# Optimization experiments

Measured on AMD Instinct MI355X. Metric: run time of the kernel, lower is better.

The kernel has to match this reference:

```python
import jax, jax.numpy as jnp
import numpy as np

NB, NLOC, DIN, DOUT = 4, 4096, 512, 512
NTYPES, TEBD = 128, 128
N_EXPERTS, TOP_K = 8, 2  # share_expert = 0 -> routed_experts = 8, routed_top_k = 2


def setup_inputs() -> dict:
    key = jax.random.key(0)
    k = jax.random.split(key, 6)
    return {
        "x": jax.random.normal(k[0], (NB, NLOC, DIN), dtype=jnp.float32),
        "type_embeddings": jax.random.normal(k[1], (NTYPES, TEBD), dtype=jnp.float32),
        "atom_types": jax.random.randint(k[2], (NB, NLOC), 0, NTYPES, dtype=jnp.int32),
        "Wg": jax.random.normal(k[3], (TEBD, N_EXPERTS), dtype=jnp.float32) / np.sqrt(TEBD),
        "We": jax.random.normal(k[4], (N_EXPERTS, DIN, DOUT), dtype=jnp.float32) / np.sqrt(DIN),
        "be": jax.random.normal(k[5], (N_EXPERTS, DOUT), dtype=jnp.float32) * 0.01,
    }


def reference(x, type_embeddings, atom_types, Wg, We, be):
    # --- route: gate on type embeddings, then index per atom (MD-continuous) ---
    logits = type_embeddings @ Wg                       # [ntypes, E]
    top_vals, top_idx = jax.lax.top_k(logits, TOP_K)    # [ntypes, K]
    weights = jax.nn.softmax(top_vals, axis=-1)         # softmax over selected logits
    atom_w = weights[atom_types]                        # [nb, nloc, K]
    atom_i = top_idx[atom_types]                        # [nb, nloc, K]

    # scatter-add top-k weights into dense per-expert weights (matches scatter_add_)
    onehot = jax.nn.one_hot(atom_i, N_EXPERTS, dtype=x.dtype)   # [nb, nloc, K, E]
    per_expert_w = jnp.einsum("bnk,bnke->bne", atom_w, onehot)  # [nb, nloc, E]

    # --- run all experts densely (the batched JIT-friendly path), then combine ---
    expert_out = jnp.tanh(jnp.einsum("bnd,edo->bneo", x, We) + be)  # [nb, nloc, E, dout]
    out = jnp.einsum("bne,bneo->bno", per_expert_w, expert_out)     # [nb, nloc, dout]
    return out
```

## Files before the change

kernel.cpp:

```cpp
#include <hip/hip_runtime.h>
#include <hip/hip_bf16.h>
#include <math.h>

typedef __bf16 bf16;
typedef __bf16 bf16x8 __attribute__((ext_vector_type(8)));
typedef float  f32x4  __attribute__((ext_vector_type(4)));

#define NTOK   16384
#define DIN    512
#define DOUT   512
#define NTYPES 128
#define TEBD   128
#define NEXP   8
#define NPAIR  64
#define MAXTILE 192

#define WS_HPART   0
#define WS_ROUTE_W 32768
#define WS_BASET   33792
#define WS_CURS    34304
#define WS_CNTP    34816
#define WS_BASEP   35072
#define WS_NTILE   35328
#define WS_TMAP    35840
#define WS_RMAP    37888
#define WS_WGT     (WS_RMAP + MAXTILE * 128 * 4)
#define WS_XB      (WS_WGT + MAXTILE * 128 * 8)
#define WS_WET     (WS_XB + (size_t)NTOK * DIN * 2)

#define GLOAD_LDS16(g, l)                                                     \
  __builtin_amdgcn_global_load_lds(                                           \
      (const __attribute__((address_space(1))) void*)(g),                     \
      (__attribute__((address_space(3))) void*)(l), 16, 0, 0)

__global__ void fused_prep_kernel(const float* __restrict__ x,
                                  const float* __restrict__ We,
                                  const int* __restrict__ atype,
                                  int* __restrict__ hpart,
                                  bf16* __restrict__ xb,
                                  bf16* __restrict__ WeT) {
  int bx = blockIdx.x;
  int tid = threadIdx.x;
  if (bx < 64) {
    __shared__ int h[NTYPES];
    if (tid < NTYPES) h[tid] = 0;
    __syncthreads();
    int t = bx * 256 + tid;
    atomicAdd(&h[atype[t]], 1);
    __syncthreads();
    if (tid < NTYPES) hpart[tid * 64 + bx] = h[tid];
  } else if (bx < 576) {
    __shared__ float t[64][65];
    int b2 = bx - 64;
    int e = b2 >> 6;
    int rem = b2 & 63;
    int kt = (rem >> 3) * 64;
    int nt = (rem & 7) * 64;
    int col = tid & 63;
    int rq = tid >> 6;
#pragma unroll
    for (int r = 0; r < 16; ++r) {
      int row = rq * 16 + r;
      t[row][col] = We[((size_t)e * DIN + kt + row) * DOUT + nt + col];
    }
    __syncthreads();
#pragma unroll
    for (int r = 0; r < 16; ++r) {
      int n = rq * 16 + r;
      WeT[((size_t)e * DOUT + nt + n) * DIN + kt + col] = (bf16)t[col][n];
    }
  } else {
    size_t base = (size_t)(bx - 576) * 4096 + tid * 16;
    const float4* p = (const float4*)(x + base);
    float4 a0 = p[0], a1 = p[1], a2 = p[2], a3 = p[3];
    bf16x8 o0, o1;
    o0[0] = (bf16)a0.x; o0[1] = (bf16)a0.y; o0[2] = (bf16)a0.z; o0[3] = (bf16)a0.w;
    o0[4] = (bf16)a1.x; o0[5] = (bf16)a1.y; o0[6] = (bf16)a1.z; o0[7] = (bf16)a1.w;
    o1[0] = (bf16)a2.x; o1[1] = (bf16)a2.y; o1[2] = (bf16)a2.z; o1[3] = (bf16)a2.w;
    o1[4] = (bf16)a3.x; o1[5] = (bf16)a3.y; o1[6] = (bf16)a3.z; o1[7] = (bf16)a3.w;
    *(bf16x8*)(xb + base) = o0;
    *(bf16x8*)(xb + base + 8) = o1;
  }
}

__global__ void route_scan_kernel(const float* __restrict__ emb,
                                  const float* __restrict__ Wg,
                                  const int* __restrict__ hpart,
                                  float* __restrict__ route_w,
                                  int* __restrict__ base_type,
                                  int* __restrict__ cursor,
                                  int* __restrict__ cnt_pair,
                                  int* __restrict__ base_pair,
                                  int* __restrict__ ntile,
                                  int* __restrict__ tmap,
                                  int* __restrict__ row_map) {
  __shared__ int s_cnt[NPAIR];
  __shared__ int s_off[NTYPES];
  __shared__ int s_pair[NTYPES];
  int t = threadIdx.x;
  if (t < NPAIR) s_cnt[t] = 0;
  __syncthreads();

  int myc = 0;
  {
    const int4* hp = (const int4*)(hpart + t * 64);
#pragma unroll
    for (int b = 0; b < 16; ++b) {
      int4 v = hp[b];
      myc += v.x + v.y + v.z + v.w;
    }
  }

  const float* er = emb + (size_t)t * TEBD;
  float lg[NEXP];
#pragma unroll
  for (int e = 0; e < NEXP; ++e) lg[e] = 0.f;
  for (int j = 0; j < TEBD; ++j) {
    float ev = er[j];
#pragma unroll
    for (int e = 0; e < NEXP; ++e) lg[e] += ev * Wg[j * NEXP + e];
  }
  float v0 = -__builtin_inff(), v1 = -__builtin_inff();
  int i0 = 0, i1 = 0;
#pragma unroll
  for (int e = 0; e < NEXP; ++e) {
    float v = lg[e];
    if (v > v0) { v1 = v0; i1 = i0; v0 = v; i0 = e; }
    else if (v > v1) { v1 = v; i1 = e; }
  }
  float d = expf(v1 - v0);
  float inv = 1.f / (1.f + d);
  route_w[t * 2 + 0] = inv;
  route_w[t * 2 + 1] = d * inv;
  int p = i0 * 8 + i1;
  s_pair[t] = p;
  s_off[t] = atomicAdd(&s_cnt[p], myc);
  cursor[t] = 0;
  __syncthreads();

  if (t < NPAIR) {
    int b = 0, tb = 0;
    for (int j = 0; j < t; ++j) {
      int nt_j = (s_cnt[j] + 127) >> 7;
      b += nt_j << 7;
      tb += nt_j;
    }
    base_pair[t] = b;
    cnt_pair[t] = s_cnt[t];
    int nt_l = (s_cnt[t] + 127) >> 7;
    for (int i = 0; i < nt_l; ++i) {
      tmap[(tb + i) * 2 + 0] = t;
      tmap[(tb + i) * 2 + 1] = i * 128;
    }
    for (int i = s_cnt[t]; i < (nt_l << 7); ++i) row_map[b + i] = 0;
    if (t == NPAIR - 1) ntile[0] = tb + nt_l;
  }
  __syncthreads();
  base_type[t] = base_pair[s_pair[t]] + s_off[t];
}

__global__ void place_kernel(const int* __restrict__ atype,
                             const float* __restrict__ route_w,
                             const int* __restrict__ base_type,
                             int* __restrict__ cursor,
                             int* __restrict__ row_map,
                             float* __restrict__ wgt) {
  __shared__ int lc[NTYPES];
  __shared__ int lb[NTYPES];
  int tid = threadIdx.x;
  if (tid < NTYPES) lc[tid] = 0;
  __syncthreads();
  int t = blockIdx.x * 256 + tid;
  int ty = atype[t];
  int r = atomicAdd(&lc[ty], 1);
  __syncthreads();
  if (tid < NTYPES) lb[tid] = lc[tid] ? atomicAdd(&cursor[tid], lc[tid]) : 0;
  __syncthreads();
  int pos = base_type[ty] + lb[ty] + r;
  row_map[pos] = t;
  ((float2*)wgt)[pos] = ((const float2*)route_w)[ty];
}

__global__ __launch_bounds__(256, 2) void moe_gemm_pair_kernel(
    const bf16* __restrict__ xb, const bf16* __restrict__ WeT,
    const float* __restrict__ be, const int* __restrict__ cnt_pair,
    const int* __restrict__ ntile, const int* __restrict__ tmap,
    const int* __restrict__ row_map, const float* __restrict__ wgt,
    float* __restrict__ out) {
  int nwork = ntile[0] * 8;
  int f = blockIdx.y * 8 + blockIdx.x;
  if (f >= nwork) return;
  int q = nwork >> 3, r = nwork & 7;
  int xcd = f & 7, idx = f >> 3;
  int L = (xcd < r ? xcd * (q + 1) : r * (q + 1) + (xcd - r) * q) + idx;
  int ti = L >> 3;
  int cx = L & 7;
  int list = tmap[ti * 2 + 0];
  int r0   = tmap[ti * 2 + 1];
  int e0 = list >> 3, e1 = list & 7;
  int nrow = cnt_pair[list] - r0;
  if (nrow > 128) nrow = 128;
  int c0 = cx * 64;
  int arow0 = ti * 128;

  __shared__ __align__(16) bf16 As[4][128 * 32];
  __shared__ __align__(16) bf16 B0s[4][64 * 32];
  __shared__ __align__(16) bf16 B1s[4][64 * 32];
  __shared__ int   tokS[128];
  __shared__ float w0S[128], w1S[128];
  __shared__ float be0S[64], be1S[64];

  int tid = threadIdx.x;
  int lane = tid & 63, w = tid >> 6;

  if (tid < 128) {
    int srow = (tid < nrow) ? tid : (nrow - 1);
    tokS[tid] = row_map[arow0 + srow];
    float2 ww = ((const float2*)wgt)[arow0 + srow];
    w0S[tid] = ww.x;
    w1S[tid] = ww.y;
    if (tid < 64) {
      be0S[tid] = be[e0 * DOUT + c0 + tid];
      be1S[tid] = be[e1 * DOUT + c0 + tid];
    }
  }
  __syncthreads();

  const bf16* srcA[2];
#pragma unroll
  for (int j = 0; j < 2; ++j) {
    int slot = w * 128 + j * 64 + lane;
    int row = slot >> 2, cs = slot & 3;
    int c = cs ^ ((row >> 1) & 3);
    srcA[j] = xb + (size_t)tokS[row] * DIN + c * 8;
  }
  const bf16* srcB0;
  const bf16* srcB1;
  {
    int slot = w * 64 + lane;
    int row = slot >> 2, cs = slot & 3;
    int c = cs ^ ((row >> 1) & 3);
    srcB0 = WeT + ((size_t)e0 * DOUT + c0 + row) * DIN + c * 8;
    srcB1 = WeT + ((size_t)e1 * DOUT + c0 + row) * DIN + c * 8;
  }

  auto stage = [&](int buf) {
#pragma unroll
    for (int j = 0; j < 2; ++j) {
      GLOAD_LDS16(srcA[j], &As[buf][(w * 128 + j * 64) * 8]);
      srcA[j] += 32;
    }
    GLOAD_LDS16(srcB0, &B0s[buf][w * 64 * 8]);
    GLOAD_LDS16(srcB1, &B1s[buf][w * 64 * 8]);
    srcB0 += 32;
    srcB1 += 32;
  };

  stage(0);
  stage(1);
  stage(2);

  f32x4 acc0[4][2], acc1[4][2];
#pragma unroll
  for (int mi = 0; mi < 4; ++mi)
#pragma unroll
    for (int ni = 0; ni < 2; ++ni) { acc0[mi][ni] = (f32x4)0.f; acc1[mi][ni] = (f32x4)0.f; }

  int wm = (w >> 1) * 64;
  int wn = (w & 1) * 32;
  int r16 = lane & 15, g16 = lane >> 4;

  int offA[4], offB[2];
#pragma unroll
  for (int i = 0; i < 4; ++i) {
    int rA = wm + i * 16 + r16;
    offA[i] = rA * 32 + (g16 ^ ((rA >> 1) & 3)) * 8;
  }
#pragma unroll
  for (int i = 0; i < 2; ++i) {
    int rB = wn + i * 16 + r16;
    offB[i] = rB * 32 + (g16 ^ ((rB >> 1) & 3)) * 8;
  }

#pragma unroll
  for (int t = 0; t < 16; ++t) {
    if (t < 14)      asm volatile("s_waitcnt vmcnt(8)" ::: "memory");
    else if (t == 14) asm volatile("s_waitcnt vmcnt(4)" ::: "memory");
    else              asm volatile("s_waitcnt vmcnt(0)" ::: "memory");
    __builtin_amdgcn_s_barrier();
    if (t + 3 < 16) stage((t + 3) & 3);

    int cur = t & 3;
    bf16x8 af[4], b0f[2], b1f[2];
#pragma unroll
    for (int i = 0; i < 4; ++i) af[i] = *(const bf16x8*)&As[cur][offA[i]];
#pragma unroll
    for (int i = 0; i < 2; ++i) b0f[i] = *(const bf16x8*)&B0s[cur][offB[i]];
#pragma unroll
    for (int i = 0; i < 2; ++i) b1f[i] = *(const bf16x8*)&B1s[cur][offB[i]];
    __builtin_amdgcn_s_setprio(1);
#pragma unroll
    for (int mi = 0; mi < 4; ++mi)
#pragma unroll
      for (int ni = 0; ni < 2; ++ni) {
        acc0[mi][ni] = __builtin_amdgcn_mfma_f32_16x16x32_bf16(
            af[mi], b0f[ni], acc0[mi][ni], 0, 0, 0);
        acc1[mi][ni] = __builtin_amdgcn_mfma_f32_16x16x32_bf16(
            af[mi], b1f[ni], acc1[mi][ni], 0, 0, 0);
      }
    __builtin_amdgcn_s_setprio(0);
  }

#pragma unroll
  for (int mi = 0; mi < 4; ++mi) {
#pragma unroll
    for (int ni = 0; ni < 2; ++ni) {
      f32x4 v0 = acc0[mi][ni];
      f32x4 v1 = acc1[mi][ni];
      int colLocal = wn + ni * 16 + r16;
      float bev0 = be0S[colLocal];
      float bev1 = be1S[colLocal];
#pragma unroll
      for (int r = 0; r < 4; ++r) {
        int lrow = wm + mi * 16 + g16 * 4 + r;
        if (lrow < nrow) {
          float x0 = fminf(9.f, fmaxf(-9.f, v0[r] + bev0)) * 2.885390082f;
          float x1 = fminf(9.f, fmaxf(-9.f, v1[r] + bev1)) * 2.885390082f;
          float e0v, e1v, invd;
          asm("v_exp_f32 %0, %1" : "=v"(e0v) : "v"(x0));
          asm("v_exp_f32 %0, %1" : "=v"(e1v) : "v"(x1));
          float d0 = e0v + 1.f, d1 = e1v + 1.f;
          asm("v_rcp_f32 %0, %1" : "=v"(invd) : "v"(d0 * d1));
          float t0 = (e0v - 1.f) * d1 * invd;
          float t1 = (e1v - 1.f) * d0 * invd;
          out[(size_t)tokS[lrow] * DOUT + c0 + colLocal] =
              t0 * w0S[lrow] + t1 * w1S[lrow];
        }
      }
    }
  }
}

extern "C" void kernel_launch(void* const* d_in, const int* in_sizes, int n_in,
                              void* d_out, int out_size, void* d_ws, size_t ws_size,
                              hipStream_t stream) {
  const float* x    = (const float*)d_in[0];
  const float* emb  = (const float*)d_in[1];
  const int*   aty  = (const int*)d_in[2];
  const float* Wg   = (const float*)d_in[3];
  const float* We   = (const float*)d_in[4];
  const float* be   = (const float*)d_in[5];
  float* out = (float*)d_out;

  char* ws = (char*)d_ws;
  int*   hpart     = (int*)(ws + WS_HPART);
  float* route_w   = (float*)(ws + WS_ROUTE_W);
  int*   base_type = (int*)(ws + WS_BASET);
  int*   cursor    = (int*)(ws + WS_CURS);
  int*   cnt_pair  = (int*)(ws + WS_CNTP);
  int*   base_pair = (int*)(ws + WS_BASEP);
  int*   ntile     = (int*)(ws + WS_NTILE);
  int*   tmap      = (int*)(ws + WS_TMAP);
  int*   row_map   = (int*)(ws + WS_RMAP);
  float* wgt       = (float*)(ws + WS_WGT);
  bf16*  xb        = (bf16*)(ws + WS_XB);
  bf16*  WeT       = (bf16*)(ws + WS_WET);

  fused_prep_kernel<<<2624, 256, 0, stream>>>(x, We, aty, hpart, xb, WeT);
  route_scan_kernel<<<1, 128, 0, stream>>>(emb, Wg, hpart, route_w, base_type,
                                           cursor, cnt_pair, base_pair, ntile,
                                           tmap, row_map);
  place_kernel<<<NTOK / 256, 256, 0, stream>>>(aty, route_w, base_type, cursor,
                                               row_map, wgt);
  moe_gemm_pair_kernel<<<dim3(8, MAXTILE), 256, 0, stream>>>(
      xb, WeT, be, cnt_pair, ntile, tmap, row_map, wgt, out);
}
```

Before: 74.83 us.

## Fuse x bf16 conversion into GEMM A-tile load; drop separate x cast pass

Removes the standalone pass that converted x to bf16 in a workspace. The GEMM now loads fp32 rows of x straight into LDS and converts them to bf16 while building fragments. The We transpose moves into the placement kernel, and the histogram becomes its own small kernel. This saves a full read and write of x, but each GEMM tile now loads twice the A bytes into LDS. To fit LDS it also drops from 4 to 3 pipeline stages, which shortens the prefetch depth.

```diff
diff --git a/kernel.cpp b/kernel.cpp
--- a/kernel.cpp
+++ b/kernel.cpp
@@ -25,62 +25,22 @@
 #define WS_TMAP    35840
 #define WS_RMAP    37888
 #define WS_WGT     (WS_RMAP + MAXTILE * 128 * 4)
-#define WS_XB      (WS_WGT + MAXTILE * 128 * 8)
-#define WS_WET     (WS_XB + (size_t)NTOK * DIN * 2)
+#define WS_WET     (WS_WGT + MAXTILE * 128 * 8)
 
 #define GLOAD_LDS16(g, l)                                                     \
   __builtin_amdgcn_global_load_lds(                                           \
       (const __attribute__((address_space(1))) void*)(g),                     \
       (__attribute__((address_space(3))) void*)(l), 16, 0, 0)
 
-__global__ void fused_prep_kernel(const float* __restrict__ x,
-                                  const float* __restrict__ We,
-                                  const int* __restrict__ atype,
-                                  int* __restrict__ hpart,
-                                  bf16* __restrict__ xb,
-                                  bf16* __restrict__ WeT) {
-  int bx = blockIdx.x;
+__global__ void hist_kernel(const int* __restrict__ atype, int* __restrict__ hpart) {
+  __shared__ int h[NTYPES];
   int tid = threadIdx.x;
-  if (bx < 64) {
-    __shared__ int h[NTYPES];
-    if (tid < NTYPES) h[tid] = 0;
-    __syncthreads();
-    int t = bx * 256 + tid;
-    atomicAdd(&h[atype[t]], 1);
-    __syncthreads();
-    if (tid < NTYPES) hpart[tid * 64 + bx] = h[tid];
-  } else if (bx < 576) {
-    __shared__ float t[64][65];
-    int b2 = bx - 64;
-    int e = b2 >> 6;
-    int rem = b2 & 63;
-    int kt = (rem >> 3) * 64;
-    int nt = (rem & 7) * 64;
-    int col = tid & 63;
-    int rq = tid >> 6;
-#pragma unroll
-    for (int r = 0; r < 16; ++r) {
-      int row = rq * 16 + r;
-      t[row][col] = We[((size_t)e * DIN + kt + row) * DOUT + nt + col];
-    }
-    __syncthreads();
-#pragma unroll
-    for (int r = 0; r < 16; ++r) {
-      int n = rq * 16 + r;
-      WeT[((size_t)e * DOUT + nt + n) * DIN + kt + col] = (bf16)t[col][n];
-    }
-  } else {
-    size_t base = (size_t)(bx - 576) * 4096 + tid * 16;
-    const float4* p = (const float4*)(x + base);
-    float4 a0 = p[0], a1 = p[1], a2 = p[2], a3 = p[3];
-    bf16x8 o0, o1;
-    o0[0] = (bf16)a0.x; o0[1] = (bf16)a0.y; o0[2] = (bf16)a0.z; o0[3] = (bf16)a0.w;
-    o0[4] = (bf16)a1.x; o0[5] = (bf16)a1.y; o0[6] = (bf16)a1.z; o0[7] = (bf16)a1.w;
-    o1[0] = (bf16)a2.x; o1[1] = (bf16)a2.y; o1[2] = (bf16)a2.z; o1[3] = (bf16)a2.w;
-    o1[4] = (bf16)a3.x; o1[5] = (bf16)a3.y; o1[6] = (bf16)a3.z; o1[7] = (bf16)a3.w;
-    *(bf16x8*)(xb + base) = o0;
-    *(bf16x8*)(xb + base + 8) = o1;
-  }
+  if (tid < NTYPES) h[tid] = 0;
+  __syncthreads();
+  int t = blockIdx.x * 256 + tid;
+  atomicAdd(&h[atype[t]], 1);
+  __syncthreads();
+  if (tid < NTYPES) hpart[tid * 64 + blockIdx.x] = h[tid];
 }
 
 __global__ void route_scan_kernel(const float* __restrict__ emb,
@@ -159,30 +119,55 @@
   base_type[t] = base_pair[s_pair[t]] + s_off[t];
 }
 
-__global__ void place_kernel(const int* __restrict__ atype,
+__global__ void prep2_kernel(const float* __restrict__ We,
+                             const int* __restrict__ atype,
                              const float* __restrict__ route_w,
                              const int* __restrict__ base_type,
                              int* __restrict__ cursor,
                              int* __restrict__ row_map,
-                             float* __restrict__ wgt) {
-  __shared__ int lc[NTYPES];
-  __shared__ int lb[NTYPES];
+                             float* __restrict__ wgt,
+                             bf16* __restrict__ WeT) {
+  int bx = blockIdx.x;
   int tid = threadIdx.x;
-  if (tid < NTYPES) lc[tid] = 0;
-  __syncthreads();
-  int t = blockIdx.x * 256 + tid;
-  int ty = atype[t];
-  int r = atomicAdd(&lc[ty], 1);
-  __syncthreads();
-  if (tid < NTYPES) lb[tid] = lc[tid] ? atomicAdd(&cursor[tid], lc[tid]) : 0;
-  __syncthreads();
-  int pos = base_type[ty] + lb[ty] + r;
-  row_map[pos] = t;
-  ((float2*)wgt)[pos] = ((const float2*)route_w)[ty];
+  if (bx < 64) {
+    __shared__ int lc[NTYPES];
+    __shared__ int lb[NTYPES];
+    if (tid < NTYPES) lc[tid] = 0;
+    __syncthreads();
+    int t = bx * 256 + tid;
+    int ty = atype[t];
+    int r = atomicAdd(&lc[ty], 1);
+    __syncthreads();
+    if (tid < NTYPES) lb[tid] = lc[tid] ? atomicAdd(&cursor[tid], lc[tid]) : 0;
+    __syncthreads();
+    int pos = base_type[ty] + lb[ty] + r;
+    row_map[pos] = t;
+    ((float2*)wgt)[pos] = ((const float2*)route_w)[ty];
+  } else {
+    __shared__ float t[64][65];
+    int b2 = bx - 64;
+    int e = b2 >> 6;
+    int rem = b2 & 63;
+    int kt = (rem >> 3) * 64;
+    int nt = (rem & 7) * 64;
+    int col = tid & 63;
+    int rq = tid >> 6;
+#pragma unroll
+    for (int r = 0; r < 16; ++r) {
+      int row = rq * 16 + r;
+      t[row][col] = We[((size_t)e * DIN + kt + row) * DOUT + nt + col];
+    }
+    __syncthreads();
+#pragma unroll
+    for (int r = 0; r < 16; ++r) {
+      int n = rq * 16 + r;
+      WeT[((size_t)e * DOUT + nt + n) * DIN + kt + col] = (bf16)t[col][n];
+    }
+  }
 }
 
 __global__ __launch_bounds__(256, 2) void moe_gemm_pair_kernel(
-    const bf16* __restrict__ xb, const bf16* __restrict__ WeT,
+    const float* __restrict__ x, const bf16* __restrict__ WeT,
     const float* __restrict__ be, const int* __restrict__ cnt_pair,
     const int* __restrict__ ntile, const int* __restrict__ tmap,
     const int* __restrict__ row_map, const float* __restrict__ wgt,
@@ -203,9 +188,9 @@
   int c0 = cx * 64;
   int arow0 = ti * 128;
 
-  __shared__ __align__(16) bf16 As[4][128 * 32];
-  __shared__ __align__(16) bf16 B0s[4][64 * 32];
-  __shared__ __align__(16) bf16 B1s[4][64 * 32];
+  __shared__ __align__(16) float Asf[3][128 * 32];
+  __shared__ __align__(16) bf16  B0s[3][64 * 32];
+  __shared__ __align__(16) bf16  B1s[3][64 * 32];
   __shared__ int   tokS[128];
   __shared__ float w0S[128], w1S[128];
   __shared__ float be0S[64], be1S[64];
@@ -226,13 +211,13 @@
   }
   __syncthreads();
 
-  const bf16* srcA[2];
-#pragma unroll
-  for (int j = 0; j < 2; ++j) {
-    int slot = w * 128 + j * 64 + lane;
-    int row = slot >> 2, cs = slot & 3;
-    int c = cs ^ ((row >> 1) & 3);
-    srcA[j] = xb + (size_t)tokS[row] * DIN + c * 8;
+  const float* srcA[4];
+#pragma unroll
+  for (int j = 0; j < 4; ++j) {
+    int slot = (j * 4 + w) * 64 + lane;
+    int row = slot >> 3, cs = slot & 7;
+    int c = cs ^ (row & 7);
+    srcA[j] = x + (size_t)tokS[row] * DIN + c * 4;
   }
   const bf16* srcB0;
   const bf16* srcB1;
@@ -246,8 +231,8 @@
 
   auto stage = [&](int buf) {
 #pragma unroll
-    for (int j = 0; j < 2; ++j) {
-      GLOAD_LDS16(srcA[j], &As[buf][(w * 128 + j * 64) * 8]);
+    for (int j = 0; j < 4; ++j) {
+      GLOAD_LDS16(srcA[j], &Asf[buf][((j * 4 + w) * 64) * 4]);
       srcA[j] += 32;
     }
     GLOAD_LDS16(srcB0, &B0s[buf][w * 64 * 8]);
@@ -258,7 +243,6 @@
 
   stage(0);
   stage(1);
-  stage(2);
 
   f32x4 acc0[4][2], acc1[4][2];
 #pragma unroll
@@ -270,11 +254,12 @@
   int wn = (w & 1) * 32;
   int r16 = lane & 15, g16 = lane >> 4;
 
-  int offA[4], offB[2];
+  int offAe[4], offAo[4], offB[2];
 #pragma unroll
   for (int i = 0; i < 4; ++i) {
     int rA = wm + i * 16 + r16;
-    offA[i] = rA * 32 + (g16 ^ ((rA >> 1) & 3)) * 8;
+    offAe[i] = rA * 32 + (((2 * g16) ^ (rA & 7)) * 4);
+    offAo[i] = rA * 32 + (((2 * g16 + 1) ^ (rA & 7)) * 4);
   }
 #pragma unroll
   for (int i = 0; i < 2; ++i) {
@@ -284,16 +269,22 @@
 
 #pragma unroll
   for (int t = 0; t < 16; ++t) {
-    if (t < 14)      asm volatile("s_waitcnt vmcnt(8)" ::: "memory");
-    else if (t == 14) asm volatile("s_waitcnt vmcnt(4)" ::: "memory");
-    else              asm volatile("s_waitcnt vmcnt(0)" ::: "memory");
+    if (t < 15) asm volatile("s_waitcnt vmcnt(6)" ::: "memory");
+    else        asm volatile("s_waitcnt vmcnt(0)" ::: "memory");
     __builtin_amdgcn_s_barrier();
-    if (t + 3 < 16) stage((t + 3) & 3);
-
-    int cur = t & 3;
+    if (t + 2 < 16) stage((t + 2) % 3);
+
+    int cur = t % 3;
     bf16x8 af[4], b0f[2], b1f[2];
 #pragma unroll
-    for (int i = 0; i < 4; ++i) af[i] = *(const bf16x8*)&As[cur][offA[i]];
+    for (int i = 0; i < 4; ++i) {
+      float4 fe = *(const float4*)&Asf[cur][offAe[i]];
+      float4 fo = *(const float4*)&Asf[cur][offAo[i]];
+      bf16x8 a;
+      a[0] = (bf16)fe.x; a[1] = (bf16)fe.y; a[2] = (bf16)fe.z; a[3] = (bf16)fe.w;
+      a[4] = (bf16)fo.x; a[5] = (bf16)fo.y; a[6] = (bf16)fo.z; a[7] = (bf16)fo.w;
+      af[i] = a;
+    }
 #pragma unroll
     for (int i = 0; i < 2; ++i) b0f[i] = *(const bf16x8*)&B0s[cur][offB[i]];
 #pragma unroll
@@ -363,15 +354,14 @@
   int*   tmap      = (int*)(ws + WS_TMAP);
   int*   row_map   = (int*)(ws + WS_RMAP);
   float* wgt       = (float*)(ws + WS_WGT);
-  bf16*  xb        = (bf16*)(ws + WS_XB);
   bf16*  WeT       = (bf16*)(ws + WS_WET);
 
-  fused_prep_kernel<<<2624, 256, 0, stream>>>(x, We, aty, hpart, xb, WeT);
+  hist_kernel<<<64, 256, 0, stream>>>(aty, hpart);
   route_scan_kernel<<<1, 128, 0, stream>>>(emb, Wg, hpart, route_w, base_type,
                                            cursor, cnt_pair, base_pair, ntile,
                                            tmap, row_map);
-  place_kernel<<<NTOK / 256, 256, 0, stream>>>(aty, route_w, base_type, cursor,
-                                               row_map, wgt);
+  prep2_kernel<<<64 + 512, 256, 0, stream>>>(We, aty, route_w, base_type,
+                                             cursor, row_map, wgt, WeT);
   moe_gemm_pair_kernel<<<dim3(8, MAXTILE), 256, 0, stream>>>(
-      xb, WeT, be, cnt_pair, ntile, tmap, row_map, wgt, out);
-}
+      x, WeT, be, cnt_pair, ntile, tmap, row_map, wgt, out);
+}
```

Measured after the change: 81.13 us. 1.08x slower.

## Merge prep, route, and place kernels into one cooperative grid-synced kernel

Applied to the files above, without the earlier changes.

Replaces three separate launches (histogram and convert, single-block route/scan, place) with one cooperative kernel of 512 blocks that uses grid.sync between phases. The routing scan overlaps with the We transpose and x bf16 conversion, which now run in grid-stride loops over 447 blocks. Atomics are used for cross-block visibility. The aim is to remove launch gaps and the serial tail of the single-block scan kernel, at the cost of grid-wide barrier overhead and fewer blocks for the bandwidth-bound conversion work.

```diff
diff --git a/kernel.cpp b/kernel.cpp
--- a/kernel.cpp
+++ b/kernel.cpp
@@ -1,6 +1,9 @@
 #include <hip/hip_runtime.h>
 #include <hip/hip_bf16.h>
+#include <hip/hip_cooperative_groups.h>
 #include <math.h>
+
+namespace cg = cooperative_groups;
 
 typedef __bf16 bf16;
 typedef __bf16 bf16x8 __attribute__((ext_vector_type(8)));
@@ -20,7 +23,6 @@
 #define WS_BASET   33792
 #define WS_CURS    34304
 #define WS_CNTP    34816
-#define WS_BASEP   35072
 #define WS_NTILE   35328
 #define WS_TMAP    35840
 #define WS_RMAP    37888
@@ -33,152 +35,147 @@
       (const __attribute__((address_space(1))) void*)(g),                     \
       (__attribute__((address_space(3))) void*)(l), 16, 0, 0)
 
-__global__ void fused_prep_kernel(const float* __restrict__ x,
-                                  const float* __restrict__ We,
-                                  const int* __restrict__ atype,
-                                  int* __restrict__ hpart,
-                                  bf16* __restrict__ xb,
-                                  bf16* __restrict__ WeT) {
-  int bx = blockIdx.x;
+__device__ __forceinline__ int aload(int* p) { return atomicAdd(p, 0); }
+
+__global__ __launch_bounds__(256) void coop_prep_kernel(
+    const float* __restrict__ x, const float* __restrict__ emb,
+    const int* __restrict__ atype, const float* __restrict__ Wg,
+    const float* __restrict__ We,
+    int* hpart, float* route_w, int* base_type, int* cursor,
+    int* cnt_pair, int* ntile, int* tmap, int* row_map, float* wgt,
+    bf16* xb, bf16* WeT) {
+  cg::grid_group grid = cg::this_grid();
+  int b = blockIdx.x;
   int tid = threadIdx.x;
-  if (bx < 64) {
-    __shared__ int h[NTYPES];
+
+  __shared__ int   h[NTYPES];
+  __shared__ float tle[64][65];
+  __shared__ int   s_cnt[NPAIR];
+  __shared__ int   s_base[NPAIR];
+  __shared__ int   s_off[NTYPES];
+  __shared__ int   s_pair[NTYPES];
+  __shared__ int   lc[NTYPES];
+  __shared__ int   lb[NTYPES];
+
+  if (b < 64) {
+    if (b == 0 && tid < NTYPES) atomicExch(&cursor[tid], 0);
     if (tid < NTYPES) h[tid] = 0;
     __syncthreads();
-    int t = bx * 256 + tid;
-    atomicAdd(&h[atype[t]], 1);
-    __syncthreads();
-    if (tid < NTYPES) hpart[tid * 64 + bx] = h[tid];
-  } else if (bx < 576) {
-    __shared__ float t[64][65];
-    int b2 = bx - 64;
-    int e = b2 >> 6;
-    int rem = b2 & 63;
-    int kt = (rem >> 3) * 64;
-    int nt = (rem & 7) * 64;
-    int col = tid & 63;
-    int rq = tid >> 6;
-#pragma unroll
-    for (int r = 0; r < 16; ++r) {
-      int row = rq * 16 + r;
-      t[row][col] = We[((size_t)e * DIN + kt + row) * DOUT + nt + col];
-    }
-    __syncthreads();
-#pragma unroll
-    for (int r = 0; r < 16; ++r) {
-      int n = rq * 16 + r;
-      WeT[((size_t)e * DOUT + nt + n) * DIN + kt + col] = (bf16)t[col][n];
-    }
-  } else {
-    size_t base = (size_t)(bx - 576) * 4096 + tid * 16;
-    const float4* p = (const float4*)(x + base);
-    float4 a0 = p[0], a1 = p[1], a2 = p[2], a3 = p[3];
-    bf16x8 o0, o1;
-    o0[0] = (bf16)a0.x; o0[1] = (bf16)a0.y; o0[2] = (bf16)a0.z; o0[3] = (bf16)a0.w;
-    o0[4] = (bf16)a1.x; o0[5] = (bf16)a1.y; o0[6] = (bf16)a1.z; o0[7] = (bf16)a1.w;
-    o1[0] = (bf16)a2.x; o1[1] = (bf16)a2.y; o1[2] = (bf16)a2.z; o1[3] = (bf16)a2.w;
-    o1[4] = (bf16)a3.x; o1[5] = (bf16)a3.y; o1[6] = (bf16)a3.z; o1[7] = (bf16)a3.w;
-    *(bf16x8*)(xb + base) = o0;
-    *(bf16x8*)(xb + base + 8) = o1;
-  }
-}
-
-__global__ void route_scan_kernel(const float* __restrict__ emb,
-                                  const float* __restrict__ Wg,
-                                  const int* __restrict__ hpart,
-                                  float* __restrict__ route_w,
-                                  int* __restrict__ base_type,
-                                  int* __restrict__ cursor,
-                                  int* __restrict__ cnt_pair,
-                                  int* __restrict__ base_pair,
-                                  int* __restrict__ ntile,
-                                  int* __restrict__ tmap,
-                                  int* __restrict__ row_map) {
-  __shared__ int s_cnt[NPAIR];
-  __shared__ int s_off[NTYPES];
-  __shared__ int s_pair[NTYPES];
-  int t = threadIdx.x;
-  if (t < NPAIR) s_cnt[t] = 0;
-  __syncthreads();
-
-  int myc = 0;
-  {
-    const int4* hp = (const int4*)(hpart + t * 64);
-#pragma unroll
-    for (int b = 0; b < 16; ++b) {
-      int4 v = hp[b];
-      myc += v.x + v.y + v.z + v.w;
-    }
-  }
-
-  const float* er = emb + (size_t)t * TEBD;
-  float lg[NEXP];
-#pragma unroll
-  for (int e = 0; e < NEXP; ++e) lg[e] = 0.f;
-  for (int j = 0; j < TEBD; ++j) {
-    float ev = er[j];
-#pragma unroll
-    for (int e = 0; e < NEXP; ++e) lg[e] += ev * Wg[j * NEXP + e];
-  }
-  float v0 = -__builtin_inff(), v1 = -__builtin_inff();
-  int i0 = 0, i1 = 0;
-#pragma unroll
-  for (int e = 0; e < NEXP; ++e) {
-    float v = lg[e];
-    if (v > v0) { v1 = v0; i1 = i0; v0 = v; i0 = e; }
-    else if (v > v1) { v1 = v; i1 = e; }
-  }
-  float d = expf(v1 - v0);
-  float inv = 1.f / (1.f + d);
-  route_w[t * 2 + 0] = inv;
-  route_w[t * 2 + 1] = d * inv;
-  int p = i0 * 8 + i1;
-  s_pair[t] = p;
-  s_off[t] = atomicAdd(&s_cnt[p], myc);
-  cursor[t] = 0;
-  __syncthreads();
-
-  if (t < NPAIR) {
-    int b = 0, tb = 0;
-    for (int j = 0; j < t; ++j) {
-      int nt_j = (s_cnt[j] + 127) >> 7;
-      b += nt_j << 7;
-      tb += nt_j;
-    }
-    base_pair[t] = b;
-    cnt_pair[t] = s_cnt[t];
-    int nt_l = (s_cnt[t] + 127) >> 7;
-    for (int i = 0; i < nt_l; ++i) {
-      tmap[(tb + i) * 2 + 0] = t;
-      tmap[(tb + i) * 2 + 1] = i * 128;
-    }
-    for (int i = s_cnt[t]; i < (nt_l << 7); ++i) row_map[b + i] = 0;
-    if (t == NPAIR - 1) ntile[0] = tb + nt_l;
-  }
-  __syncthreads();
-  base_type[t] = base_pair[s_pair[t]] + s_off[t];
-}
-
-__global__ void place_kernel(const int* __restrict__ atype,
-                             const float* __restrict__ route_w,
-                             const int* __restrict__ base_type,
-                             int* __restrict__ cursor,
-                             int* __restrict__ row_map,
-                             float* __restrict__ wgt) {
-  __shared__ int lc[NTYPES];
-  __shared__ int lb[NTYPES];
-  int tid = threadIdx.x;
-  if (tid < NTYPES) lc[tid] = 0;
-  __syncthreads();
-  int t = blockIdx.x * 256 + tid;
-  int ty = atype[t];
-  int r = atomicAdd(&lc[ty], 1);
-  __syncthreads();
-  if (tid < NTYPES) lb[tid] = lc[tid] ? atomicAdd(&cursor[tid], lc[tid]) : 0;
-  __syncthreads();
-  int pos = base_type[ty] + lb[ty] + r;
-  row_map[pos] = t;
-  ((float2*)wgt)[pos] = ((const float2*)route_w)[ty];
+    atomicAdd(&h[atype[b * 256 + tid]], 1);
+    __syncthreads();
+    if (tid < NTYPES) atomicExch(&hpart[tid * 64 + b], h[tid]);
+  }
+  grid.sync();
+
+  if (b == 64) {
+    int t = tid;
+    if (t < NPAIR) s_cnt[t] = 0;
+    __syncthreads();
+    int myc = 0, i0 = 0, i1 = 0;
+    float inv = 0.f, d = 0.f;
+    if (t < NTYPES) {
+      for (int bb = 0; bb < 64; ++bb) myc += aload(&hpart[t * 64 + bb]);
+      const float* er = emb + (size_t)t * TEBD;
+      float lg[NEXP];
+#pragma unroll
+      for (int e = 0; e < NEXP; ++e) lg[e] = 0.f;
+      for (int j = 0; j < TEBD; ++j) {
+        float ev = er[j];
+#pragma unroll
+        for (int e = 0; e < NEXP; ++e) lg[e] += ev * Wg[j * NEXP + e];
+      }
+      float v0 = -__builtin_inff(), v1 = -__builtin_inff();
+#pragma unroll
+      for (int e = 0; e < NEXP; ++e) {
+        float v = lg[e];
+        if (v > v0) { v1 = v0; i1 = i0; v0 = v; i0 = e; }
+        else if (v > v1) { v1 = v; i1 = e; }
+      }
+      d = expf(v1 - v0);
+      inv = 1.f / (1.f + d);
+      int p = i0 * 8 + i1;
+      s_pair[t] = p;
+      s_off[t] = atomicAdd(&s_cnt[p], myc);
+    }
+    __syncthreads();
+    if (t < NPAIR) {
+      int bb = 0, tb = 0;
+      for (int j = 0; j < t; ++j) {
+        int nt_j = (s_cnt[j] + 127) >> 7;
+        bb += nt_j << 7;
+        tb += nt_j;
+      }
+      s_base[t] = bb;
+      cnt_pair[t] = s_cnt[t];
+      int nt_l = (s_cnt[t] + 127) >> 7;
+      for (int i = 0; i < nt_l; ++i) {
+        tmap[(tb + i) * 2 + 0] = t;
+        tmap[(tb + i) * 2 + 1] = i * 128;
+      }
+      for (int i = s_cnt[t]; i < (nt_l << 7); ++i) row_map[bb + i] = 0;
+      if (t == NPAIR - 1) ntile[0] = tb + nt_l;
+    }
+    __syncthreads();
+    if (t < NTYPES) {
+      atomicExch(&base_type[t], s_base[s_pair[t]] + s_off[t]);
+      atomicExch((int*)&route_w[t * 2 + 0], __float_as_int(inv));
+      atomicExch((int*)&route_w[t * 2 + 1], __float_as_int(d * inv));
+    }
+  } else if (b >= 65) {
+    int wj = b - 65;
+    for (int job = wj; job < 512; job += 447) {
+      int e = job >> 6;
+      int rem = job & 63;
+      int kt = (rem >> 3) * 64;
+      int nt = (rem & 7) * 64;
+      int col = tid & 63;
+      int rq = tid >> 6;
+#pragma unroll
+      for (int r = 0; r < 16; ++r) {
+        int row = rq * 16 + r;
+        tle[row][col] = We[((size_t)e * DIN + kt + row) * DOUT + nt + col];
+      }
+      __syncthreads();
+#pragma unroll
+      for (int r = 0; r < 16; ++r) {
+        int n = rq * 16 + r;
+        WeT[((size_t)e * DOUT + nt + n) * DIN + kt + col] = (bf16)tle[col][n];
+      }
+      __syncthreads();
+    }
+    for (size_t j = (size_t)wj * 256 + tid; j < (size_t)NTOK * DIN / 16;
+         j += 447 * 256) {
+      size_t base = j * 16;
+      const float4* p = (const float4*)(x + base);
+      float4 a0 = p[0], a1 = p[1], a2 = p[2], a3 = p[3];
+      bf16x8 o0, o1;
+      o0[0] = (bf16)a0.x; o0[1] = (bf16)a0.y; o0[2] = (bf16)a0.z; o0[3] = (bf16)a0.w;
+      o0[4] = (bf16)a1.x; o0[5] = (bf16)a1.y; o0[6] = (bf16)a1.z; o0[7] = (bf16)a1.w;
+      o1[0] = (bf16)a2.x; o1[1] = (bf16)a2.y; o1[2] = (bf16)a2.z; o1[3] = (bf16)a2.w;
+      o1[4] = (bf16)a3.x; o1[5] = (bf16)a3.y; o1[6] = (bf16)a3.z; o1[7] = (bf16)a3.w;
+      *(bf16x8*)(xb + base) = o0;
+      *(bf16x8*)(xb + base + 8) = o1;
+    }
+  }
+  grid.sync();
+
+  if (b < 64) {
+    if (tid < NTYPES) lc[tid] = 0;
+    __syncthreads();
+    int t = b * 256 + tid;
+    int ty = atype[t];
+    int r = atomicAdd(&lc[ty], 1);
+    __syncthreads();
+    if (tid < NTYPES) lb[tid] = lc[tid] ? atomicAdd(&cursor[tid], lc[tid]) : 0;
+    __syncthreads();
+    int bt = aload(&base_type[ty]);
+    int pos = bt + lb[ty] + r;
+    row_map[pos] = t;
+    float w0 = __int_as_float(aload((int*)&route_w[ty * 2 + 0]));
+    float w1 = __int_as_float(aload((int*)&route_w[ty * 2 + 1]));
+    float2 ww; ww.x = w0; ww.y = w1;
+    ((float2*)wgt)[pos] = ww;
+  }
 }
 
 __global__ __launch_bounds__(256, 2) void moe_gemm_pair_kernel(
@@ -358,7 +355,6 @@
   int*   base_type = (int*)(ws + WS_BASET);
   int*   cursor    = (int*)(ws + WS_CURS);
   int*   cnt_pair  = (int*)(ws + WS_CNTP);
-  int*   base_pair = (int*)(ws + WS_BASEP);
   int*   ntile     = (int*)(ws + WS_NTILE);
   int*   tmap      = (int*)(ws + WS_TMAP);
   int*   row_map   = (int*)(ws + WS_RMAP);
@@ -366,12 +362,13 @@
   bf16*  xb        = (bf16*)(ws + WS_XB);
   bf16*  WeT       = (bf16*)(ws + WS_WET);
 
-  fused_prep_kernel<<<2624, 256, 0, stream>>>(x, We, aty, hpart, xb, WeT);
-  route_scan_kernel<<<1, 128, 0, stream>>>(emb, Wg, hpart, route_w, base_type,
-                                           cursor, cnt_pair, base_pair, ntile,
-                                           tmap, row_map);
-  place_kernel<<<NTOK / 256, 256, 0, stream>>>(aty, route_w, base_type, cursor,
-                                               row_map, wgt);
+  void* args[] = {
+      (void*)&x, (void*)&emb, (void*)&aty, (void*)&Wg, (void*)&We,
+      (void*)&hpart, (void*)&route_w, (void*)&base_type, (void*)&cursor,
+      (void*)&cnt_pair, (void*)&ntile, (void*)&tmap, (void*)&row_map,
+      (void*)&wgt, (void*)&xb, (void*)&WeT};
+  hipLaunchCooperativeKernel((const void*)coop_prep_kernel, dim3(512),
+                             dim3(256), args, 0, stream);
   moe_gemm_pair_kernel<<<dim3(8, MAXTILE), 256, 0, stream>>>(
       xb, WeT, be, cnt_pair, ntile, tmap, row_map, wgt, out);
 }
```

Measured after the change: 203.3 us. +171.7%, slower.
